# Kernel tuning notes

Hardware: AMD Instinct MI355X
Metric: run time of the kernel (lower is better)

Reference implementation:

```python
import jax, jax.numpy as jnp
import numpy as np

CHANNELS = 512
NUM_HEADS = 8


def setup_inputs() -> dict:
    key = jax.random.key(0)
    ks = jax.random.split(key, 5)
    c = CHANNELS
    x = jax.random.normal(ks[0], (8, c, 32, 32), dtype=jnp.float32)
    # nn.Linear(channels, 3*channels) weight is (out, in); keep torch layout
    w_qkv = jax.random.normal(ks[1], (3 * c, c), dtype=jnp.float32) / np.sqrt(c)
    b_qkv = jax.random.normal(ks[2], (3 * c,), dtype=jnp.float32) * 0.01
    w_o = jax.random.normal(ks[3], (c, c), dtype=jnp.float32) / np.sqrt(c)
    b_o = jax.random.normal(ks[4], (c,), dtype=jnp.float32) * 0.01
    return {"x": x, "w_qkv": w_qkv, "b_qkv": b_qkv, "w_o": w_o, "b_o": b_o}


def reference(x, w_qkv, b_qkv, w_o, b_o):
    b, c, h, w = x.shape
    nh = NUM_HEADS
    hd = c // nh
    # b c h w -> b (h w) c
    xs = jnp.transpose(x.reshape(b, c, h * w), (0, 2, 1))  # [b, s, c]
    qkv = xs @ w_qkv.T + b_qkv                              # [b, s, 3c]
    q, k, v = qkv[..., :c], qkv[..., c:2 * c], qkv[..., 2 * c:]
    s = h * w
    q = q.reshape(b, s, nh, hd).transpose(0, 2, 1, 3)       # [b, nh, s, hd]
    k = k.reshape(b, s, nh, hd).transpose(0, 2, 1, 3)
    v = v.reshape(b, s, nh, hd).transpose(0, 2, 1, 3)
    scores = jnp.einsum('bnqd,bnkd->bnqk', q, k) / np.sqrt(hd).astype(np.float32)
    probs = jax.nn.softmax(scores, axis=-1)                 # [b, nh, s, s]
    av = jnp.einsum('bnqk,bnkd->bqnd', probs, v).reshape(b, s, c)
    out = av @ w_o.T + b_o                                  # [b, s, c]
    # b (h w) c -> b c h w
    return jnp.transpose(out, (0, 2, 1)).reshape(b, c, h, w)
```

## Files before the change

kernel.cpp:

```cpp
#include <hip/hip_runtime.h>
#include <cstddef>
#include <cstdint>

#define CH 512
#define SEQ 1024
#define NH 8
#define HD 64

typedef unsigned short u16;
typedef unsigned int u32;
typedef __attribute__((ext_vector_type(8))) short bf16x8;
typedef __attribute__((ext_vector_type(4))) float f32x4;
typedef __attribute__((ext_vector_type(4))) unsigned short u16x4;

#define SCLQ 0.1803368801111204f

__device__ __forceinline__ u16 f2bf(float f) {
  unsigned u = __float_as_uint(f);
  u += 0x7fffu + ((u >> 16) & 1u);
  return (u16)(u >> 16);
}
__device__ __forceinline__ float bf2f(u16 h) {
  return __uint_as_float(((unsigned)h) << 16);
}
__device__ __forceinline__ u32 cvtpk(float lo, float hi) {
  u32 r;
  asm("v_cvt_pk_bf16_f32 %0, %1, %2" : "=v"(r) : "v"(lo), "v"(hi));
  return r;
}

__device__ __forceinline__ void gld16(void* lds, const void* g) {
  __builtin_amdgcn_global_load_lds(
      (const __attribute__((address_space(1))) unsigned int*)g,
      (__attribute__((address_space(3))) unsigned int*)lds, 16, 0, 0);
}

__device__ __forceinline__ f32x4 mfma16(bf16x8 a, bf16x8 b, f32x4 c) {
  return __builtin_amdgcn_mfma_f32_16x16x32_bf16(a, b, c, 0, 0, 0);
}

__global__ __launch_bounds__(256) void split_plain(
    const float* __restrict__ in, u16* __restrict__ hi, u16* __restrict__ lo, int n4)
{
  int i = blockIdx.x * 256 + threadIdx.x;
  if (i < n4) {
    float4 v = ((const float4*)in)[i];
    float vv0 = v.x, vv1 = v.y, vv2 = v.z, vv3 = v.w;
    u16x4 h, l;
    h[0] = f2bf(vv0); l[0] = f2bf(vv0 - bf2f(h[0]));
    h[1] = f2bf(vv1); l[1] = f2bf(vv1 - bf2f(h[1]));
    h[2] = f2bf(vv2); l[2] = f2bf(vv2 - bf2f(h[2]));
    h[3] = f2bf(vv3); l[3] = f2bf(vv3 - bf2f(h[3]));
    ((u16x4*)hi)[i] = h;
    ((u16x4*)lo)[i] = l;
  }
}

__global__ __launch_bounds__(256) void transpose_split(
    const float* __restrict__ x, u16* __restrict__ xh, u16* __restrict__ xl)
{
  __shared__ float tile[64][65];
  const int s0 = blockIdx.x * 64, c0 = blockIdx.y * 64, bz = blockIdx.z;
  const int t = threadIdx.x;
  #pragma unroll
  for (int p = 0; p < 16; ++p) {
    int i = p * 256 + t;
    int cl = i >> 6, sl = i & 63;
    tile[cl][sl] = x[((size_t)bz * CH + c0 + cl) * SEQ + s0 + sl];
  }
  __syncthreads();
  #pragma unroll
  for (int p = 0; p < 16; ++p) {
    int i = p * 256 + t;
    int sl = i >> 6, cl = i & 63;
    float v = tile[cl][sl];
    u16 h = f2bf(v);
    size_t idx = ((size_t)bz * SEQ + s0 + sl) * CH + c0 + cl;
    xh[idx] = h;
    xl[idx] = f2bf(v - bf2f(h));
  }
}

template<int MODE, int BM>
__global__ __launch_bounds__(256, 2) void gemm_hilo(
    const u16* __restrict__ Ah, const u16* __restrict__ Al,
    const u16* __restrict__ BTh, const u16* __restrict__ BTl,
    const float* __restrict__ bias,
    void* __restrict__ o0, void* __restrict__ o1, void* __restrict__ o2,
    void* __restrict__ o3, void* __restrict__ o4)
{
  constexpr int WM = BM / 2;
  constexpr int MI = WM / 16;
  const int bx = blockIdx.x, by = blockIdx.y, bz = blockIdx.z;
  const int m0 = by * BM, n0 = bx * 128;
  const char* Ahc = (const char*)Ah;
  const char* Alc = (const char*)Al;
  const char* Bhc = (const char*)BTh + (size_t)bz * SEQ * CH * 2;
  const char* Blc = (const char*)BTl + (size_t)bz * SEQ * CH * 2;

  __shared__ __align__(16) u16 As[BM * 64];
  __shared__ __align__(16) u16 Bs[128 * 64];

  const int t = threadIdx.x, w = t >> 6, lane = t & 63;
  const int lr = lane & 15, lg = lane >> 4;
  const int wr = w >> 1, wc = w & 1;

  f32x4 acc[MI][4];
  #pragma unroll
  for (int i = 0; i < MI; ++i)
    #pragma unroll
    for (int j = 0; j < 4; ++j) acc[i][j] = (f32x4){0.f, 0.f, 0.f, 0.f};

  for (int k0 = 0; k0 < CH; k0 += 32) {
    __syncthreads();
    #pragma unroll
    for (int p = 0; p < BM / 32; ++p) {
      const int ldsoff = p * 4096 + w * 1024 + lane * 16;
      const int m = ldsoff >> 7;
      const int W = ldsoff & 127;
      const int Wp = W ^ ((m & 7) << 4);
      const char* src = (Wp < 64 ? Ahc : Alc) + ((size_t)(m0 + m) * CH + k0) * 2 + (Wp & 63);
      gld16((char*)As + p * 4096 + w * 1024, src);
    }
    #pragma unroll
    for (int p = 0; p < 4; ++p) {
      const int ldsoff = p * 4096 + w * 1024 + lane * 16;
      const int n = ldsoff >> 7;
      const int W = ldsoff & 127;
      const int Wp = W ^ ((n & 7) << 4);
      const char* src = (Wp < 64 ? Bhc : Blc) + ((size_t)(n0 + n) * CH + k0) * 2 + (Wp & 63);
      gld16((char*)Bs + p * 4096 + w * 1024, src);
    }
    __syncthreads();

    bf16x8 Afh[MI], Afl[MI], Bfh[4], Bfl[4];
    #pragma unroll
    for (int mi = 0; mi < MI; ++mi) {
      const int m = wr * WM + mi * 16 + lr;
      const int swz = (m & 7) << 4;
      Afh[mi] = *(const bf16x8*)((const char*)As + m * 128 + ((lg * 16) ^ swz));
      Afl[mi] = *(const bf16x8*)((const char*)As + m * 128 + ((64 + lg * 16) ^ swz));
    }
    #pragma unroll
    for (int ni = 0; ni < 4; ++ni) {
      const int n = wc * 64 + ni * 16 + lr;
      const int swz = (n & 7) << 4;
      Bfh[ni] = *(const bf16x8*)((const char*)Bs + n * 128 + ((lg * 16) ^ swz));
      Bfl[ni] = *(const bf16x8*)((const char*)Bs + n * 128 + ((64 + lg * 16) ^ swz));
    }
    #pragma unroll
    for (int mi = 0; mi < MI; ++mi) {
      #pragma unroll
      for (int ni = 0; ni < 4; ++ni) {
        acc[mi][ni] = mfma16(Afh[mi], Bfh[ni], acc[mi][ni]);
        acc[mi][ni] = mfma16(Afh[mi], Bfl[ni], acc[mi][ni]);
        acc[mi][ni] = mfma16(Afl[mi], Bfh[ni], acc[mi][ni]);
      }
    }
  }

  if constexpr (MODE == 0) {
    float* Out = (float*)o0 + (size_t)bz * CH * SEQ;
    #pragma unroll
    for (int mi = 0; mi < MI; ++mi) {
      const int mb = m0 + wr * WM + mi * 16 + lg * 4;
      #pragma unroll
      for (int r = 0; r < 4; ++r) {
        const float bv = bias[mb + r];
        #pragma unroll
        for (int ni = 0; ni < 4; ++ni) {
          const int n = n0 + wc * 64 + ni * 16 + lr;
          Out[(size_t)(mb + r) * SEQ + n] = acc[mi][ni][r] + bv;
        }
      }
    }
  } else {
    u16* qh = (u16*)o0; u16* ql = (u16*)o1;
    u16* kh = (u16*)o2;
    u16* vh = (u16*)o4;
    #pragma unroll
    for (int mi = 0; mi < MI; ++mi) {
      const int mb = m0 + wr * WM + mi * 16 + lg * 4;
      const int sec = mb >> 9;
      const int h = (mb >> 6) & 7;
      const int d = mb & 63;
      const size_t bh = (size_t)bz * NH + h;
      const float b0 = bias[mb + 0], b1 = bias[mb + 1], b2 = bias[mb + 2], b3 = bias[mb + 3];
      #pragma unroll
      for (int ni = 0; ni < 4; ++ni) {
        const int n = n0 + wc * 64 + ni * 16 + lr;
        float c0 = acc[mi][ni][0] + b0;
        float c1 = acc[mi][ni][1] + b1;
        float c2 = acc[mi][ni][2] + b2;
        float c3 = acc[mi][ni][3] + b3;
        if (sec == 2) {
          u16* dst = vh + (bh * HD + d) * SEQ + n;
          dst[0 * SEQ] = f2bf(c0);
          dst[1 * SEQ] = f2bf(c1);
          dst[2 * SEQ] = f2bf(c2);
          dst[3 * SEQ] = f2bf(c3);
        } else if (sec == 1) {
          u16* dsth = kh + (bh * SEQ + n) * HD + d;
          u16x4 hv;
          hv[0] = f2bf(c0); hv[1] = f2bf(c1); hv[2] = f2bf(c2); hv[3] = f2bf(c3);
          *(u16x4*)dsth = hv;
        } else {
          c0 *= SCLQ; c1 *= SCLQ; c2 *= SCLQ; c3 *= SCLQ;
          u16* dsth = qh + (bh * SEQ + n) * HD + d;
          u16* dstl = ql + (bh * SEQ + n) * HD + d;
          u16x4 hv, lv;
          hv[0] = f2bf(c0); lv[0] = f2bf(c0 - bf2f(hv[0]));
          hv[1] = f2bf(c1); lv[1] = f2bf(c1 - bf2f(hv[1]));
          hv[2] = f2bf(c2); lv[2] = f2bf(c2 - bf2f(hv[2]));
          hv[3] = f2bf(c3); lv[3] = f2bf(c3 - bf2f(hv[3]));
          *(u16x4*)dsth = hv;
          *(u16x4*)dstl = lv;
        }
      }
    }
  }
}

__global__ __launch_bounds__(256, 4) void attn_mfma(
    const u16* __restrict__ q_h, const u16* __restrict__ q_l,
    const u16* __restrict__ k_h, const u16* __restrict__ v_h,
    u16* __restrict__ av_h, u16* __restrict__ av_l)
{
  const int bid = blockIdx.x;
  const int xcd = bid & 7, rr = bid >> 3;
  const int qt = rr & 15, ghi = rr >> 4;
  const int g = ghi * 8 + xcd;
  const int hh = g & 7, bz = g >> 3;
  const int bhead = bz * NH + hh;
  const int s0 = qt * 64;
  const int t = threadIdx.x, w = t >> 6, lane = t & 63;
  const int lr = lane & 15, lg = lane >> 4;
  const int gsw = ((lr & 7) << 4) | (lr & 8);

  __shared__ __align__(16) u16 KsH[2][4096];
  __shared__ __align__(16) u16 Vs[2][4096];
  __shared__ __align__(16) u16 Ps[4][1024];

  bf16x8 QBh[2], QBl[2];
  {
    const size_t qrow = (size_t)bhead * SEQ + s0 + w * 16 + lr;
    #pragma unroll
    for (int ks = 0; ks < 2; ++ks) {
      QBh[ks] = *(const bf16x8*)((const char*)q_h + qrow * 128 + ks * 64 + lg * 16);
      QBl[ks] = *(const bf16x8*)((const char*)q_l + qrow * 128 + ks * 64 + lg * 16);
    }
  }

  const char* Khb = (const char*)k_h + (size_t)bhead * SEQ * 128;
  const char* Vbb = (const char*)v_h + (size_t)bhead * HD * 2048;

  auto STAGE = [&](int buf, int tile) {
    const char* ks = Khb + (size_t)tile * 8192;
    const char* vsrc = Vbb + (size_t)tile * 128;
    #pragma unroll
    for (int p = 0; p < 2; ++p) {
      const int ldsoff = w * 2048 + p * 1024 + lane * 16;
      const int r = ldsoff >> 7;
      const int Wp = (ldsoff & 127) ^ ((r & 7) << 4);
      gld16((char*)KsH[buf] + ldsoff, ks + r * 128 + Wp);
      gld16((char*)Vs[buf] + ldsoff, vsrc + (size_t)r * 2048 + Wp);
    }
  };

  float mreg = -1e30f, lreg = 0.f;
  f32x4 oacc[4];
  #pragma unroll
  for (int ni = 0; ni < 4; ++ni) oacc[ni] = (f32x4){0.f, 0.f, 0.f, 0.f};

  STAGE(0, 0);
  __syncthreads();

  for (int kt = 0; kt < 16; ++kt) {
    const int cur = kt & 1;
    if (kt < 15) STAGE(cur ^ 1, kt + 1);

    f32x4 sc[4];
    #pragma unroll
    for (int ni = 0; ni < 4; ++ni) sc[ni] = (f32x4){0.f, 0.f, 0.f, 0.f};
    #pragma unroll
    for (int ks = 0; ks < 2; ++ks) {
      bf16x8 kf[4];
      #pragma unroll
      for (int ni = 0; ni < 4; ++ni) {
        const int row = ni * 16 + lr;
        kf[ni] = *(const bf16x8*)((const char*)KsH[cur] + row * 128 +
                                  ((ks * 64 + lg * 16) ^ ((row & 7) << 4)));
      }
      __builtin_amdgcn_s_setprio(1);
      #pragma unroll
      for (int ni = 0; ni < 4; ++ni) {
        sc[ni] = mfma16(kf[ni], QBh[ks], sc[ni]);
        sc[ni] = mfma16(kf[ni], QBl[ks], sc[ni]);
      }
      __builtin_amdgcn_s_setprio(0);
    }

    float tm = fmaxf(fmaxf(sc[0][0], sc[0][1]), fmaxf(sc[0][2], sc[0][3]));
    #pragma unroll
    for (int ni = 1; ni < 4; ++ni)
      tm = fmaxf(tm, fmaxf(fmaxf(sc[ni][0], sc[ni][1]), fmaxf(sc[ni][2], sc[ni][3])));
    tm = fmaxf(tm, __shfl_xor(tm, 16));
    tm = fmaxf(tm, __shfl_xor(tm, 32));

    if (!__all(tm <= mreg + 8.0f)) {
      const float mn = fmaxf(mreg, tm);
      const float alv = exp2f(mreg - mn);
      mreg = mn;
      lreg *= alv;
      float alr[4];
      #pragma unroll
      for (int r = 0; r < 4; ++r) alr[r] = __shfl(alv, lg * 4 + r);
      #pragma unroll
      for (int ni = 0; ni < 4; ++ni)
        #pragma unroll
        for (int r = 0; r < 4; ++r) oacc[ni][r] *= alr[r];
    }

    char* Pw = (char*)Ps[w] + lr * 128;
    #pragma unroll
    for (int ni = 0; ni < 4; ++ni) {
      const float p0 = exp2f(sc[ni][0] - mreg);
      const float p1 = exp2f(sc[ni][1] - mreg);
      const float p2 = exp2f(sc[ni][2] - mreg);
      const float p3 = exp2f(sc[ni][3] - mreg);
      lreg += (p0 + p1) + (p2 + p3);
      *(uint2*)(Pw + ((ni * 32 + lg * 8) ^ gsw)) =
          make_uint2(cvtpk(p0, p1), cvtpk(p2, p3));
    }

    #pragma unroll
    for (int ks = 0; ks < 2; ++ks) {
      bf16x8 vb[4];
      #pragma unroll
      for (int ni = 0; ni < 4; ++ni) {
        const int d = ni * 16 + lr;
        vb[ni] = *(const bf16x8*)((const char*)Vs[cur] + d * 128 +
                                  ((ks * 64 + lg * 16) ^ ((d & 7) << 4)));
      }
      const uint2 a = *(const uint2*)(Pw + ((ks * 64 + lg * 16 + 0) ^ gsw));
      const uint2 b = *(const uint2*)(Pw + ((ks * 64 + lg * 16 + 8) ^ gsw));
      union { u32 u[4]; bf16x8 v; } pu;
      pu.u[0] = a.x; pu.u[1] = a.y; pu.u[2] = b.x; pu.u[3] = b.y;
      __builtin_amdgcn_s_setprio(1);
      #pragma unroll
      for (int ni = 0; ni < 4; ++ni)
        oacc[ni] = mfma16(pu.v, vb[ni], oacc[ni]);
      __builtin_amdgcn_s_setprio(0);
    }

    __syncthreads();
  }

  float lt = lreg + __shfl_xor(lreg, 16);
  lt += __shfl_xor(lt, 32);
  const float inv = 1.f / lt;
  #pragma unroll
  for (int r = 0; r < 4; ++r) {
    const float invr = __shfl(inv, lg * 4 + r);
    const int s = s0 + w * 16 + lg * 4 + r;
    #pragma unroll
    for (int ni = 0; ni < 4; ++ni) {
      const int c = hh * HD + ni * 16 + lr;
      const size_t idx = ((size_t)bz * SEQ + s) * CH + c;
      const float v = oacc[ni][r] * invr;
      const u16 hb = f2bf(v);
      av_h[idx] = hb;
      av_l[idx] = f2bf(v - bf2f(hb));
    }
  }
}

extern "C" void kernel_launch(void* const* d_in, const int* in_sizes, int n_in,
                              void* d_out, int out_size, void* d_ws, size_t ws_size,
                              hipStream_t stream) {
  const float* x     = (const float*)d_in[0];
  const float* w_qkv = (const float*)d_in[1];
  const float* b_qkv = (const float*)d_in[2];
  const float* w_o   = (const float*)d_in[3];
  const float* b_o   = (const float*)d_in[4];
  float* out = (float*)d_out;

  char* ws = (char*)d_ws;
  const size_t SZ = (size_t)8 * SEQ * CH * 2;
  u16* xt_h = (u16*)(ws + 0 * SZ);
  u16* xt_l = (u16*)(ws + 1 * SZ);
  u16* q_h  = (u16*)(ws + 2 * SZ);
  u16* q_l  = (u16*)(ws + 3 * SZ);
  u16* k_h  = (u16*)(ws + 4 * SZ);
  u16* v_h  = (u16*)(ws + 6 * SZ);
  u16* wqkv_h = (u16*)(ws + 7 * SZ);
  u16* wqkv_l = wqkv_h + (size_t)1536 * 512;
  u16* wo_h   = wqkv_l + (size_t)1536 * 512;
  u16* wo_l   = wo_h + (size_t)512 * 512;

  split_plain<<<768, 256, 0, stream>>>(w_qkv, wqkv_h, wqkv_l, (1536 * 512) / 4);
  split_plain<<<256, 256, 0, stream>>>(w_o, wo_h, wo_l, (512 * 512) / 4);
  transpose_split<<<dim3(16, 8, 8), 256, 0, stream>>>(x, xt_h, xt_l);

  gemm_hilo<1, 128><<<dim3(8, 12, 8), 256, 0, stream>>>(
      wqkv_h, wqkv_l, xt_h, xt_l, b_qkv,
      (void*)q_h, (void*)q_l, (void*)k_h, nullptr, (void*)v_h);

  attn_mfma<<<dim3(1024), 256, 0, stream>>>(
      q_h, q_l, k_h, v_h, xt_h, xt_l);

  gemm_hilo<0, 64><<<dim3(8, 8, 8), 256, 0, stream>>>(
      wo_h, wo_l, xt_h, xt_l, b_o,
      (void*)out, nullptr, nullptr, nullptr, nullptr);
}
```

Measured before the change: 185.6 us.

## Merge weight split kernels and compute softmax row sums via MFMA

The two weight hi/lo split launches become one kernel with 1024 blocks, removing one launch. In attention the shared arrays are merged into one byte buffer with LDS addresses precomputed outside the loop, and the key loop is fully unrolled. The softmax denominator is now accumulated with an extra MFMA against a ones vector instead of scalar adds and cross-lane shuffles. This makes the sum use the bf16-rounded probabilities, which matches the PV product, and costs one more MFMA per k-step plus possible register pressure from full unrolling.

```diff
diff --git a/kernel.cpp b/kernel.cpp
--- a/kernel.cpp
+++ b/kernel.cpp
@@ -39,21 +39,22 @@
   return __builtin_amdgcn_mfma_f32_16x16x32_bf16(a, b, c, 0, 0, 0);
 }
 
-__global__ __launch_bounds__(256) void split_plain(
-    const float* __restrict__ in, u16* __restrict__ hi, u16* __restrict__ lo, int n4)
+__global__ __launch_bounds__(256) void split_both(
+    const float* __restrict__ wqkv, u16* __restrict__ wqkv_h, u16* __restrict__ wqkv_l,
+    const float* __restrict__ wo, u16* __restrict__ wo_h, u16* __restrict__ wo_l)
 {
-  int i = blockIdx.x * 256 + threadIdx.x;
-  if (i < n4) {
-    float4 v = ((const float4*)in)[i];
-    float vv0 = v.x, vv1 = v.y, vv2 = v.z, vv3 = v.w;
-    u16x4 h, l;
-    h[0] = f2bf(vv0); l[0] = f2bf(vv0 - bf2f(h[0]));
-    h[1] = f2bf(vv1); l[1] = f2bf(vv1 - bf2f(h[1]));
-    h[2] = f2bf(vv2); l[2] = f2bf(vv2 - bf2f(h[2]));
-    h[3] = f2bf(vv3); l[3] = f2bf(vv3 - bf2f(h[3]));
-    ((u16x4*)hi)[i] = h;
-    ((u16x4*)lo)[i] = l;
-  }
+  const int b = blockIdx.x;
+  const float* in; u16* hi; u16* lo; int i;
+  if (b < 768) { in = wqkv; hi = wqkv_h; lo = wqkv_l; i = b * 256 + threadIdx.x; }
+  else         { in = wo;   hi = wo_h;   lo = wo_l;   i = (b - 768) * 256 + threadIdx.x; }
+  float4 v = ((const float4*)in)[i];
+  u16x4 h, l;
+  h[0] = f2bf(v.x); l[0] = f2bf(v.x - bf2f(h[0]));
+  h[1] = f2bf(v.y); l[1] = f2bf(v.y - bf2f(h[1]));
+  h[2] = f2bf(v.z); l[2] = f2bf(v.z - bf2f(h[2]));
+  h[3] = f2bf(v.w); l[3] = f2bf(v.w - bf2f(h[3]));
+  ((u16x4*)hi)[i] = h;
+  ((u16x4*)lo)[i] = l;
 }
 
 __global__ __launch_bounds__(256) void transpose_split(
@@ -237,9 +238,7 @@
   const int lr = lane & 15, lg = lane >> 4;
   const int gsw = ((lr & 7) << 4) | (lr & 8);
 
-  __shared__ __align__(16) u16 KsH[2][4096];
-  __shared__ __align__(16) u16 Vs[2][4096];
-  __shared__ __align__(16) u16 Ps[4][1024];
+  __shared__ __align__(16) char SH[40960];
 
   bf16x8 QBh[2], QBl[2];
   {
@@ -254,20 +253,43 @@
   const char* Khb = (const char*)k_h + (size_t)bhead * SEQ * 128;
   const char* Vbb = (const char*)v_h + (size_t)bhead * HD * 2048;
 
+  const char* kp[2][4];
+  #pragma unroll
+  for (int ks = 0; ks < 2; ++ks)
+    #pragma unroll
+    for (int ni = 0; ni < 4; ++ni) {
+      const int row = ni * 16 + lr;
+      kp[ks][ni] = SH + row * 128 + ((ks * 64 + lg * 16) ^ ((row & 7) << 4));
+    }
+  char* pwp = SH + 32768 + w * 2048 + lr * 128;
+  char* pw[4];
+  #pragma unroll
+  for (int ni = 0; ni < 4; ++ni) pw[ni] = pwp + ((ni * 32 + lg * 8) ^ gsw);
+  const char* pr[2][2];
+  #pragma unroll
+  for (int ks = 0; ks < 2; ++ks)
+    #pragma unroll
+    for (int h2 = 0; h2 < 2; ++h2)
+      pr[ks][h2] = pwp + ((ks * 64 + lg * 16 + h2 * 8) ^ gsw);
+
   auto STAGE = [&](int buf, int tile) {
-    const char* ks = Khb + (size_t)tile * 8192;
+    const char* ksrc = Khb + (size_t)tile * 8192;
     const char* vsrc = Vbb + (size_t)tile * 128;
     #pragma unroll
     for (int p = 0; p < 2; ++p) {
       const int ldsoff = w * 2048 + p * 1024 + lane * 16;
       const int r = ldsoff >> 7;
       const int Wp = (ldsoff & 127) ^ ((r & 7) << 4);
-      gld16((char*)KsH[buf] + ldsoff, ks + r * 128 + Wp);
-      gld16((char*)Vs[buf] + ldsoff, vsrc + (size_t)r * 2048 + Wp);
+      gld16(SH + buf * 8192 + ldsoff, ksrc + r * 128 + Wp);
+      gld16(SH + 16384 + buf * 8192 + ldsoff, vsrc + (size_t)r * 2048 + Wp);
     }
   };
 
-  float mreg = -1e30f, lreg = 0.f;
+  union { u32 u[4]; bf16x8 v; } ones;
+  ones.u[0] = ones.u[1] = ones.u[2] = ones.u[3] = 0x3f803f80u;
+
+  float mreg = -1e30f;
+  f32x4 ls = (f32x4){0.f, 0.f, 0.f, 0.f};
   f32x4 oacc[4];
   #pragma unroll
   for (int ni = 0; ni < 4; ++ni) oacc[ni] = (f32x4){0.f, 0.f, 0.f, 0.f};
@@ -275,6 +297,7 @@
   STAGE(0, 0);
   __syncthreads();
 
+  #pragma unroll
   for (int kt = 0; kt < 16; ++kt) {
     const int cur = kt & 1;
     if (kt < 15) STAGE(cur ^ 1, kt + 1);
@@ -286,11 +309,8 @@
     for (int ks = 0; ks < 2; ++ks) {
       bf16x8 kf[4];
       #pragma unroll
-      for (int ni = 0; ni < 4; ++ni) {
-        const int row = ni * 16 + lr;
-        kf[ni] = *(const bf16x8*)((const char*)KsH[cur] + row * 128 +
-                                  ((ks * 64 + lg * 16) ^ ((row & 7) << 4)));
-      }
+      for (int ni = 0; ni < 4; ++ni)
+        kf[ni] = *(const bf16x8*)(kp[ks][ni] + cur * 8192);
       __builtin_amdgcn_s_setprio(1);
       #pragma unroll
       for (int ni = 0; ni < 4; ++ni) {
@@ -311,7 +331,6 @@
       const float mn = fmaxf(mreg, tm);
       const float alv = exp2f(mreg - mn);
       mreg = mn;
-      lreg *= alv;
       float alr[4];
       #pragma unroll
       for (int r = 0; r < 4; ++r) alr[r] = __shfl(alv, lg * 4 + r);
@@ -319,49 +338,43 @@
       for (int ni = 0; ni < 4; ++ni)
         #pragma unroll
         for (int r = 0; r < 4; ++r) oacc[ni][r] *= alr[r];
-    }
-
-    char* Pw = (char*)Ps[w] + lr * 128;
+      #pragma unroll
+      for (int r = 0; r < 4; ++r) ls[r] *= alr[r];
+    }
+
     #pragma unroll
     for (int ni = 0; ni < 4; ++ni) {
       const float p0 = exp2f(sc[ni][0] - mreg);
       const float p1 = exp2f(sc[ni][1] - mreg);
       const float p2 = exp2f(sc[ni][2] - mreg);
       const float p3 = exp2f(sc[ni][3] - mreg);
-      lreg += (p0 + p1) + (p2 + p3);
-      *(uint2*)(Pw + ((ni * 32 + lg * 8) ^ gsw)) =
-          make_uint2(cvtpk(p0, p1), cvtpk(p2, p3));
+      *(uint2*)pw[ni] = make_uint2(cvtpk(p0, p1), cvtpk(p2, p3));
     }
 
     #pragma unroll
     for (int ks = 0; ks < 2; ++ks) {
       bf16x8 vb[4];
       #pragma unroll
-      for (int ni = 0; ni < 4; ++ni) {
-        const int d = ni * 16 + lr;
-        vb[ni] = *(const bf16x8*)((const char*)Vs[cur] + d * 128 +
-                                  ((ks * 64 + lg * 16) ^ ((d & 7) << 4)));
-      }
-      const uint2 a = *(const uint2*)(Pw + ((ks * 64 + lg * 16 + 0) ^ gsw));
-      const uint2 b = *(const uint2*)(Pw + ((ks * 64 + lg * 16 + 8) ^ gsw));
+      for (int ni = 0; ni < 4; ++ni)
+        vb[ni] = *(const bf16x8*)(kp[ks][ni] + 16384 + cur * 8192);
+      const uint2 a = *(const uint2*)pr[ks][0];
+      const uint2 b = *(const uint2*)pr[ks][1];
       union { u32 u[4]; bf16x8 v; } pu;
       pu.u[0] = a.x; pu.u[1] = a.y; pu.u[2] = b.x; pu.u[3] = b.y;
       __builtin_amdgcn_s_setprio(1);
       #pragma unroll
       for (int ni = 0; ni < 4; ++ni)
         oacc[ni] = mfma16(pu.v, vb[ni], oacc[ni]);
+      ls = mfma16(pu.v, ones.v, ls);
       __builtin_amdgcn_s_setprio(0);
     }
 
     __syncthreads();
   }
 
-  float lt = lreg + __shfl_xor(lreg, 16);
-  lt += __shfl_xor(lt, 32);
-  const float inv = 1.f / lt;
   #pragma unroll
   for (int r = 0; r < 4; ++r) {
-    const float invr = __shfl(inv, lg * 4 + r);
+    const float invr = 1.f / ls[r];
     const int s = s0 + w * 16 + lg * 4 + r;
     #pragma unroll
     for (int ni = 0; ni < 4; ++ni) {
@@ -398,8 +411,7 @@
   u16* wo_h   = wqkv_l + (size_t)1536 * 512;
   u16* wo_l   = wo_h + (size_t)512 * 512;
 
-  split_plain<<<768, 256, 0, stream>>>(w_qkv, wqkv_h, wqkv_l, (1536 * 512) / 4);
-  split_plain<<<256, 256, 0, stream>>>(w_o, wo_h, wo_l, (512 * 512) / 4);
+  split_both<<<1024, 256, 0, stream>>>(w_qkv, wqkv_h, wqkv_l, w_o, wo_h, wo_l);
   transpose_split<<<dim3(16, 8, 8), 256, 0, stream>>>(x, xt_h, xt_l);
 
   gemm_hilo<1, 128><<<dim3(8, 12, 8), 256, 0, stream>>>(
```

Measured after the change: 182.8 us. About the same (-1.5%).
